# Kernel optimization log

Hardware: AMD Instinct MI355X
Metric: run time of the kernel (lower is better)

## Reference

```python
import jax, jax.numpy as jnp
import numpy as np

N_NODES = 50000
N_EDGES = 625000
IN_DIM = 128
OUT_DIM = 128


def setup_inputs() -> dict:
    key = jax.random.key(0)
    ks = jax.random.split(key, 8)
    feats = jax.random.normal(ks[0], (N_NODES, IN_DIM), dtype=jnp.float32)
    src = jax.random.randint(ks[1], (N_EDGES,), 0, N_NODES, dtype=jnp.int64)
    dst = jax.random.randint(ks[2], (N_EDGES,), 0, N_NODES, dtype=jnp.int64)
    # nn.Linear default init: U(-1/sqrt(fan_in), 1/sqrt(fan_in))
    bf = 1.0 / np.sqrt(IN_DIM)
    W_f = jax.random.uniform(ks[3], (OUT_DIM, IN_DIM), jnp.float32, -bf, bf)
    b_f = jax.random.uniform(ks[4], (OUT_DIM,), jnp.float32, -bf, bf)
    bp = 1.0 / np.sqrt(OUT_DIM)
    W_phy = jax.random.uniform(ks[5], (OUT_DIM, OUT_DIM), jnp.float32, -bp, bp)
    b_phy = jax.random.uniform(ks[6], (OUT_DIM,), jnp.float32, -bp, bp)
    eps = jnp.zeros((1,), dtype=jnp.float32)  # init_eps = 0
    return {"feats": feats, "src": src, "dst": dst, "W_f": W_f, "b_f": b_f,
            "W_phy": W_phy, "b_phy": b_phy, "eps": eps}


def reference(feats, src, dst, W_f, b_f, W_phy, b_phy, eps):
    # mlp_f (num_mlps=1): linear + relu
    h = jax.nn.relu(feats @ W_f.T + b_f)              # [N, out_dim]
    # update_all(copy_u('h'), sum): sum messages h[src] at dst
    n = jax.ops.segment_sum(h[src], dst, num_segments=N_NODES)  # [N, out_dim]
    # faithful to source: h = 1 + eps * h + n
    h = 1.0 + eps * h + n
    # mlp_phy (num_mlps=1): linear + relu
    h = jax.nn.relu(h @ W_phy.T + b_phy)
    return h
```

## Files before the change

kernel.cpp:

```cpp
#include <hip/hip_runtime.h>

#define N_NODES 50000
#define N_EDGES 625000
#define DIM 128
#define CAP 64

typedef __bf16 bf16x8 __attribute__((ext_vector_type(8)));
typedef __bf16 bf16x4 __attribute__((ext_vector_type(4)));
typedef __bf16 bf16x2 __attribute__((ext_vector_type(2)));
typedef float f32x4 __attribute__((ext_vector_type(4)));

__device__ __forceinline__ float bflo(unsigned u) { return __uint_as_float(u << 16); }
__device__ __forceinline__ float bfhi(unsigned u) { return __uint_as_float(u & 0xffff0000u); }

__global__ __launch_bounds__(512) void gemm1_fill_k(
    const float* __restrict__ A_f32,
    const float* __restrict__ W,
    const float* __restrict__ bias,
    __bf16* __restrict__ out_bf16,
    const int* __restrict__ src,
    const int* __restrict__ dst,
    int* __restrict__ cnt,
    int* __restrict__ bucket,
    const float* __restrict__ W_phy,
    __bf16* __restrict__ Wb,
    int gemm_blocks)
{
    const int t = threadIdx.x;

    if ((int)blockIdx.x >= gemm_blocks) {
        if ((int)blockIdx.x == gemm_blocks) {
            if (t < 16) {
                bf16x8 z = {};
                *(bf16x8*)&out_bf16[(size_t)N_NODES * DIM + t * 8] = z;
            }
            for (int i = t; i < 4096; i += 512) {
                float4 f = ((const float4*)W_phy)[i];
                bf16x4 pk = { (__bf16)f.x, (__bf16)f.y, (__bf16)f.z, (__bf16)f.w };
                *(bf16x4*)&Wb[i * 4] = pk;
            }
        }
        int idx = ((int)blockIdx.x - gemm_blocks) * 512 + t;
        if (idx < N_EDGES / 8) {
            int4 sa = ((const int4*)src)[idx * 2];
            int4 sb = ((const int4*)src)[idx * 2 + 1];
            int4 da = ((const int4*)dst)[idx * 2];
            int4 db = ((const int4*)dst)[idx * 2 + 1];
            int p0 = atomicAdd(&cnt[da.x], 1);
            int p1 = atomicAdd(&cnt[da.y], 1);
            int p2 = atomicAdd(&cnt[da.z], 1);
            int p3 = atomicAdd(&cnt[da.w], 1);
            int p4 = atomicAdd(&cnt[db.x], 1);
            int p5 = atomicAdd(&cnt[db.y], 1);
            int p6 = atomicAdd(&cnt[db.z], 1);
            int p7 = atomicAdd(&cnt[db.w], 1);
            bucket[(da.x << 6) + p0] = sa.x;
            bucket[(da.y << 6) + p1] = sa.y;
            bucket[(da.z << 6) + p2] = sa.z;
            bucket[(da.w << 6) + p3] = sa.w;
            bucket[(db.x << 6) + p4] = sb.x;
            bucket[(db.y << 6) + p5] = sb.y;
            bucket[(db.z << 6) + p6] = sb.z;
            bucket[(db.w << 6) + p7] = sb.w;
        }
        return;
    }

    __shared__ __align__(16) __bf16 w_lds[128 * 136];

    for (int i = t; i < 4096; i += 512) {
        float4 f = ((const float4*)W)[i];
        int n = i >> 5;
        int k = (i & 31) << 2;
        bf16x4 pk = { (__bf16)f.x, (__bf16)f.y, (__bf16)f.z, (__bf16)f.w };
        *(bf16x4*)&w_lds[n * 136 + k] = pk;
    }
    __syncthreads();

    const int wave = t >> 6;
    const int lane = t & 63;
    const int q = lane >> 4;
    const int mr = lane & 15;

    const int m0 = blockIdx.x * 128 + wave * 16;
    int arow = m0 + mr;
    if (arow >= N_NODES) arow = N_NODES - 1;

    f32x4 acc[8] = {};

#pragma unroll
    for (int ks = 0; ks < 4; ++ks) {
        const int k0 = ks * 32 + q * 8;
        const float4* ap = (const float4*)&A_f32[(size_t)arow * DIM + k0];
        float4 a0 = ap[0], a1 = ap[1];
        bf16x8 af;
        af[0] = (__bf16)a0.x; af[1] = (__bf16)a0.y;
        af[2] = (__bf16)a0.z; af[3] = (__bf16)a0.w;
        af[4] = (__bf16)a1.x; af[5] = (__bf16)a1.y;
        af[6] = (__bf16)a1.z; af[7] = (__bf16)a1.w;
#pragma unroll
        for (int nt = 0; nt < 8; ++nt) {
            bf16x8 bfr = *(const bf16x8*)&w_lds[(nt * 16 + mr) * 136 + k0];
            acc[nt] = __builtin_amdgcn_mfma_f32_16x16x32_bf16(af, bfr, acc[nt], 0, 0, 0);
        }
    }

    __syncthreads();
    float* lds_f = (float*)w_lds;
    const int nb = blockIdx.x * 128;

#pragma unroll
    for (int half = 0; half < 2; ++half) {
        if ((wave >> 2) == half) {
            int lw = wave & 3;
#pragma unroll
            for (int nt = 0; nt < 8; ++nt)
#pragma unroll
                for (int r = 0; r < 4; ++r)
                    lds_f[(lw * 16 + q * 4 + r) * 132 + nt * 16 + mr] = acc[nt][r];
        }
        __syncthreads();
        for (int i = t; i < 2048; i += 512) {
            int lr = i >> 5;
            int cg = (i & 31) << 2;
            int grow = nb + half * 64 + lr;
            if (grow < N_NODES) {
                float4 v = *(const float4*)&lds_f[lr * 132 + cg];
                float4 b4 = *(const float4*)&bias[cg];
                bf16x4 o;
                o[0] = (__bf16)fmaxf(v.x + b4.x, 0.f);
                o[1] = (__bf16)fmaxf(v.y + b4.y, 0.f);
                o[2] = (__bf16)fmaxf(v.z + b4.z, 0.f);
                o[3] = (__bf16)fmaxf(v.w + b4.w, 0.f);
                *(bf16x4*)&out_bf16[(size_t)grow * DIM + cg] = o;
            }
        }
        __syncthreads();
    }
}

__global__ __launch_bounds__(512, 4) void agg_gemm2_k(
    const __bf16* __restrict__ h,
    const int* __restrict__ cnt,
    const int* __restrict__ bucket,
    const float* __restrict__ eps_p,
    const __bf16* __restrict__ Wb,
    const float* __restrict__ bias,
    float* __restrict__ out)
{
    __shared__ __align__(16) __bf16 lds[2 * 128 * 136];
    __bf16* const w_lds = lds;
    __bf16* const a_lds = lds + 128 * 136;

    const int t = threadIdx.x;

    for (int i = t; i < 2048; i += 512) {
        int n = i >> 4;
        int kk = (i & 15) << 3;
        bf16x8 v = *(const bf16x8*)&Wb[n * DIM + kk];
        *(bf16x8*)&w_lds[n * 136 + kk] = v;
    }

    const int wave = t >> 6;
    const int lane = t & 63;
    const int ch = lane << 1;
    const int rowbase = __builtin_amdgcn_readfirstlane(blockIdx.x * 128 + wave * 16);
    const float eps = eps_p[0];

    int degv[16];
    int idxv[16];
#pragma unroll
    for (int i = 0; i < 16; ++i) {
        const int node = rowbase + i;
        const bool ok = node < N_NODES;
        degv[i] = ok ? cnt[node] : 0;
        idxv[i] = ok ? bucket[(node << 6) | lane] : N_NODES;
    }

#pragma unroll
    for (int i = 0; i < 16; ++i) {
        const int node = rowbase + i;
        const int nd = (node < N_NODES) ? node : N_NODES;
        const int deg = degv[i];
        const unsigned sv = *(const unsigned*)&h[(size_t)nd * DIM + ch];
        const int s = (lane < deg) ? idxv[i] : N_NODES;
        float ax = 0.f, ay = 0.f;
        for (int e = 0; e < deg; e += 8) {
            int s0 = __builtin_amdgcn_readlane(s, e + 0);
            int s1 = __builtin_amdgcn_readlane(s, e + 1);
            int s2 = __builtin_amdgcn_readlane(s, e + 2);
            int s3 = __builtin_amdgcn_readlane(s, e + 3);
            int s4 = __builtin_amdgcn_readlane(s, e + 4);
            int s5 = __builtin_amdgcn_readlane(s, e + 5);
            int s6 = __builtin_amdgcn_readlane(s, e + 6);
            int s7 = __builtin_amdgcn_readlane(s, e + 7);
            unsigned v0 = *(const unsigned*)&h[(size_t)s0 * DIM + ch];
            unsigned v1 = *(const unsigned*)&h[(size_t)s1 * DIM + ch];
            unsigned v2 = *(const unsigned*)&h[(size_t)s2 * DIM + ch];
            unsigned v3 = *(const unsigned*)&h[(size_t)s3 * DIM + ch];
            unsigned v4 = *(const unsigned*)&h[(size_t)s4 * DIM + ch];
            unsigned v5 = *(const unsigned*)&h[(size_t)s5 * DIM + ch];
            unsigned v6 = *(const unsigned*)&h[(size_t)s6 * DIM + ch];
            unsigned v7 = *(const unsigned*)&h[(size_t)s7 * DIM + ch];
            ax += (bflo(v0) + bflo(v1)) + (bflo(v2) + bflo(v3))
                + (bflo(v4) + bflo(v5)) + (bflo(v6) + bflo(v7));
            ay += (bfhi(v0) + bfhi(v1)) + (bfhi(v2) + bfhi(v3))
                + (bfhi(v4) + bfhi(v5)) + (bfhi(v6) + bfhi(v7));
        }
        ax = 1.0f + eps * bflo(sv) + ax;
        ay = 1.0f + eps * bfhi(sv) + ay;
        bf16x2 o; o[0] = (__bf16)ax; o[1] = (__bf16)ay;
        *(bf16x2*)&a_lds[(wave * 16 + i) * 136 + ch] = o;
    }

    __syncthreads();

    const int q = lane >> 4;
    const int mr = lane & 15;

    f32x4 acc[8] = {};

#pragma unroll
    for (int ks = 0; ks < 4; ++ks) {
        const int k0 = ks * 32 + q * 8;
        bf16x8 af = *(const bf16x8*)&a_lds[(wave * 16 + mr) * 136 + k0];
#pragma unroll
        for (int nt = 0; nt < 8; ++nt) {
            bf16x8 bfr = *(const bf16x8*)&w_lds[(nt * 16 + mr) * 136 + k0];
            acc[nt] = __builtin_amdgcn_mfma_f32_16x16x32_bf16(af, bfr, acc[nt], 0, 0, 0);
        }
    }

    __syncthreads();
    float* lds_f = (float*)lds;
    const int nb = blockIdx.x * 128;

#pragma unroll
    for (int half = 0; half < 2; ++half) {
        if ((wave >> 2) == half) {
            int lw = wave & 3;
#pragma unroll
            for (int nt = 0; nt < 8; ++nt)
#pragma unroll
                for (int r = 0; r < 4; ++r)
                    lds_f[(lw * 16 + q * 4 + r) * 132 + nt * 16 + mr] = acc[nt][r];
        }
        __syncthreads();
        for (int i2 = t; i2 < 2048; i2 += 512) {
            int lr = i2 >> 5;
            int cg = (i2 & 31) << 2;
            int grow = nb + half * 64 + lr;
            if (grow < N_NODES) {
                float4 v = *(const float4*)&lds_f[lr * 132 + cg];
                float4 b4 = *(const float4*)&bias[cg];
                v.x = fmaxf(v.x + b4.x, 0.f);
                v.y = fmaxf(v.y + b4.y, 0.f);
                v.z = fmaxf(v.z + b4.z, 0.f);
                v.w = fmaxf(v.w + b4.w, 0.f);
                *(float4*)&out[(size_t)grow * DIM + cg] = v;
            }
        }
        __syncthreads();
    }
}

extern "C" void kernel_launch(void* const* d_in, const int* in_sizes, int n_in,
                              void* d_out, int out_size, void* d_ws, size_t ws_size,
                              hipStream_t stream) {
    const float* feats = (const float*)d_in[0];
    const int*   src   = (const int*)d_in[1];
    const int*   dst   = (const int*)d_in[2];
    const float* W_f   = (const float*)d_in[3];
    const float* b_f   = (const float*)d_in[4];
    const float* W_phy = (const float*)d_in[5];
    const float* b_phy = (const float*)d_in[6];
    const float* eps   = (const float*)d_in[7];
    float* out = (float*)d_out;

    const size_t HN = (size_t)(N_NODES + 1) * DIM;
    __bf16* h   = (__bf16*)d_ws;
    int* bucket = (int*)(h + HN);
    int* cnt    = bucket + (size_t)N_NODES * CAP;
    __bf16* Wb  = (__bf16*)(cnt + N_NODES);

    const int gblocks = (N_NODES + 127) / 128;
    const int fblocks = (N_EDGES / 8 + 511) / 512;

    hipMemsetAsync(cnt, 0, N_NODES * sizeof(int), stream);

    gemm1_fill_k<<<gblocks + fblocks, 512, 0, stream>>>(
        feats, W_f, b_f, h, src, dst, cnt, bucket, W_phy, Wb, gblocks);

    agg_gemm2_k<<<gblocks, 512, 0, stream>>>(
        h, cnt, bucket, eps, Wb, b_phy, out);
}
```

Measured before the change: 152.6 us.

## Split edge bucketing into per-XCD counters with overflow buckets and LDS index compaction

The edge-bucket fill now keeps a separate counter and small 16-slot bucket per XCD for each destination node, read from the hardware XCC_ID register. Entries past that capacity go to a shared overflow bucket with its own atomic counter. The aggregation kernel ballots and compacts the eight per-XCD bucket slices and the overflow entries into a per-wave LDS index list, and prefetches the next node's metadata one step ahead. The aim is to keep atomic contention and cache-line traffic local to each XCD, at the cost of a larger memset, more metadata reads and LDS writes per node.

```diff
diff --git a/kernel.cpp b/kernel.cpp
--- a/kernel.cpp
+++ b/kernel.cpp
@@ -3,7 +3,8 @@
 #define N_NODES 50000
 #define N_EDGES 625000
 #define DIM 128
-#define CAP 64
+#define RCAP 16
+#define OCAP 64
 
 typedef __bf16 bf16x8 __attribute__((ext_vector_type(8)));
 typedef __bf16 bf16x4 __attribute__((ext_vector_type(4)));
@@ -20,8 +21,9 @@
     __bf16* __restrict__ out_bf16,
     const int* __restrict__ src,
     const int* __restrict__ dst,
-    int* __restrict__ cnt,
+    int* __restrict__ cnt9,
     int* __restrict__ bucket,
+    int* __restrict__ obucket,
     const float* __restrict__ W_phy,
     __bf16* __restrict__ Wb,
     int gemm_blocks)
@@ -40,28 +42,41 @@
                 *(bf16x4*)&Wb[i * 4] = pk;
             }
         }
+        int xcd;
+        asm volatile("s_getreg_b32 %0, hwreg(HW_REG_XCC_ID)" : "=s"(xcd));
+        xcd &= 7;
+        const int cb = xcd * N_NODES;
+
         int idx = ((int)blockIdx.x - gemm_blocks) * 512 + t;
         if (idx < N_EDGES / 8) {
             int4 sa = ((const int4*)src)[idx * 2];
             int4 sb = ((const int4*)src)[idx * 2 + 1];
             int4 da = ((const int4*)dst)[idx * 2];
             int4 db = ((const int4*)dst)[idx * 2 + 1];
-            int p0 = atomicAdd(&cnt[da.x], 1);
-            int p1 = atomicAdd(&cnt[da.y], 1);
-            int p2 = atomicAdd(&cnt[da.z], 1);
-            int p3 = atomicAdd(&cnt[da.w], 1);
-            int p4 = atomicAdd(&cnt[db.x], 1);
-            int p5 = atomicAdd(&cnt[db.y], 1);
-            int p6 = atomicAdd(&cnt[db.z], 1);
-            int p7 = atomicAdd(&cnt[db.w], 1);
-            bucket[(da.x << 6) + p0] = sa.x;
-            bucket[(da.y << 6) + p1] = sa.y;
-            bucket[(da.z << 6) + p2] = sa.z;
-            bucket[(da.w << 6) + p3] = sa.w;
-            bucket[(db.x << 6) + p4] = sb.x;
-            bucket[(db.y << 6) + p5] = sb.y;
-            bucket[(db.z << 6) + p6] = sb.z;
-            bucket[(db.w << 6) + p7] = sb.w;
+            int p0 = atomicAdd(&cnt9[cb + da.x], 1);
+            int p1 = atomicAdd(&cnt9[cb + da.y], 1);
+            int p2 = atomicAdd(&cnt9[cb + da.z], 1);
+            int p3 = atomicAdd(&cnt9[cb + da.w], 1);
+            int p4 = atomicAdd(&cnt9[cb + db.x], 1);
+            int p5 = atomicAdd(&cnt9[cb + db.y], 1);
+            int p6 = atomicAdd(&cnt9[cb + db.z], 1);
+            int p7 = atomicAdd(&cnt9[cb + db.w], 1);
+            if (p0 < RCAP) bucket[((cb + da.x) << 4) + p0] = sa.x;
+            else { int q = atomicAdd(&cnt9[8 * N_NODES + da.x], 1); obucket[(da.x << 6) + q] = sa.x; }
+            if (p1 < RCAP) bucket[((cb + da.y) << 4) + p1] = sa.y;
+            else { int q = atomicAdd(&cnt9[8 * N_NODES + da.y], 1); obucket[(da.y << 6) + q] = sa.y; }
+            if (p2 < RCAP) bucket[((cb + da.z) << 4) + p2] = sa.z;
+            else { int q = atomicAdd(&cnt9[8 * N_NODES + da.z], 1); obucket[(da.z << 6) + q] = sa.z; }
+            if (p3 < RCAP) bucket[((cb + da.w) << 4) + p3] = sa.w;
+            else { int q = atomicAdd(&cnt9[8 * N_NODES + da.w], 1); obucket[(da.w << 6) + q] = sa.w; }
+            if (p4 < RCAP) bucket[((cb + db.x) << 4) + p4] = sb.x;
+            else { int q = atomicAdd(&cnt9[8 * N_NODES + db.x], 1); obucket[(db.x << 6) + q] = sb.x; }
+            if (p5 < RCAP) bucket[((cb + db.y) << 4) + p5] = sb.y;
+            else { int q = atomicAdd(&cnt9[8 * N_NODES + db.y], 1); obucket[(db.y << 6) + q] = sb.y; }
+            if (p6 < RCAP) bucket[((cb + db.z) << 4) + p6] = sb.z;
+            else { int q = atomicAdd(&cnt9[8 * N_NODES + db.z], 1); obucket[(db.z << 6) + q] = sb.z; }
+            if (p7 < RCAP) bucket[((cb + db.w) << 4) + p7] = sb.w;
+            else { int q = atomicAdd(&cnt9[8 * N_NODES + db.w], 1); obucket[(db.w << 6) + q] = sb.w; }
         }
         return;
     }
@@ -141,14 +156,16 @@
 
 __global__ __launch_bounds__(512, 4) void agg_gemm2_k(
     const __bf16* __restrict__ h,
-    const int* __restrict__ cnt,
+    const int* __restrict__ cnt9,
     const int* __restrict__ bucket,
+    const int* __restrict__ obucket,
     const float* __restrict__ eps_p,
     const __bf16* __restrict__ Wb,
     const float* __restrict__ bias,
     float* __restrict__ out)
 {
     __shared__ __align__(16) __bf16 lds[2 * 128 * 136];
+    __shared__ __align__(16) int widx_all[8][200];
     __bf16* const w_lds = lds;
     __bf16* const a_lds = lds + 128 * 136;
 
@@ -164,51 +181,68 @@
     const int wave = t >> 6;
     const int lane = t & 63;
     const int ch = lane << 1;
+    const int xq = lane >> 4;
+    const int sj = lane & 15;
     const int rowbase = __builtin_amdgcn_readfirstlane(blockIdx.x * 128 + wave * 16);
     const float eps = eps_p[0];
-
-    int degv[16];
-    int idxv[16];
+    int* const widx = widx_all[wave];
+
+    int ndv[2], cAv[2], cBv[2], rAv[2], rBv[2], ocv[2];
+    unsigned svv[2];
+    auto nload = [&](int sl, int ii) {
+        const int node = rowbase + ii;
+        const int nd = (node < N_NODES) ? node : (N_NODES - 1);
+        ndv[sl] = nd;
+        int ca = cnt9[xq * N_NODES + nd];
+        int cb = cnt9[(xq + 4) * N_NODES + nd];
+        cAv[sl] = (ca < RCAP) ? ca : RCAP;
+        cBv[sl] = (cb < RCAP) ? cb : RCAP;
+        rAv[sl] = bucket[((xq * N_NODES + nd) << 4) + sj];
+        rBv[sl] = bucket[(((xq + 4) * N_NODES + nd) << 4) + sj];
+        ocv[sl] = cnt9[8 * N_NODES + nd];
+        svv[sl] = *(const unsigned*)&h[(size_t)nd * DIM + ch];
+    };
+    nload(0, 0);
+
 #pragma unroll
     for (int i = 0; i < 16; ++i) {
-        const int node = rowbase + i;
-        const bool ok = node < N_NODES;
-        degv[i] = ok ? cnt[node] : 0;
-        idxv[i] = ok ? bucket[(node << 6) | lane] : N_NODES;
-    }
-
-#pragma unroll
-    for (int i = 0; i < 16; ++i) {
-        const int node = rowbase + i;
-        const int nd = (node < N_NODES) ? node : N_NODES;
-        const int deg = degv[i];
-        const unsigned sv = *(const unsigned*)&h[(size_t)nd * DIM + ch];
-        const int s = (lane < deg) ? idxv[i] : N_NODES;
+        if (i < 15) nload((i + 1) & 1, i + 1);
+        const int sl = i & 1;
+        const int nd = ndv[sl];
+
+        const unsigned long long mA = __ballot(sj < cAv[sl]);
+        const unsigned long long mB = __ballot(sj < cBv[sl]);
+        const unsigned long long below = (1ull << lane) - 1ull;
+        const int tA = __popcll(mA);
+        int deg = tA + __popcll(mB);
+        if (sj < cAv[sl]) widx[__popcll(mA & below)] = rAv[sl];
+        if (sj < cBv[sl]) widx[tA + __popcll(mB & below)] = rBv[sl];
+        const int oc = ocv[sl];
+        if (oc > 0) {
+            if (lane < oc) widx[deg + lane] = obucket[(nd << 6) + lane];
+            deg += oc;
+        }
+        if (lane < 8) widx[deg + lane] = N_NODES;
+
         float ax = 0.f, ay = 0.f;
         for (int e = 0; e < deg; e += 8) {
-            int s0 = __builtin_amdgcn_readlane(s, e + 0);
-            int s1 = __builtin_amdgcn_readlane(s, e + 1);
-            int s2 = __builtin_amdgcn_readlane(s, e + 2);
-            int s3 = __builtin_amdgcn_readlane(s, e + 3);
-            int s4 = __builtin_amdgcn_readlane(s, e + 4);
-            int s5 = __builtin_amdgcn_readlane(s, e + 5);
-            int s6 = __builtin_amdgcn_readlane(s, e + 6);
-            int s7 = __builtin_amdgcn_readlane(s, e + 7);
-            unsigned v0 = *(const unsigned*)&h[(size_t)s0 * DIM + ch];
-            unsigned v1 = *(const unsigned*)&h[(size_t)s1 * DIM + ch];
-            unsigned v2 = *(const unsigned*)&h[(size_t)s2 * DIM + ch];
-            unsigned v3 = *(const unsigned*)&h[(size_t)s3 * DIM + ch];
-            unsigned v4 = *(const unsigned*)&h[(size_t)s4 * DIM + ch];
-            unsigned v5 = *(const unsigned*)&h[(size_t)s5 * DIM + ch];
-            unsigned v6 = *(const unsigned*)&h[(size_t)s6 * DIM + ch];
-            unsigned v7 = *(const unsigned*)&h[(size_t)s7 * DIM + ch];
+            int4 w0 = *(const int4*)&widx[e];
+            int4 w1 = *(const int4*)&widx[e + 4];
+            unsigned v0 = *(const unsigned*)&h[(size_t)w0.x * DIM + ch];
+            unsigned v1 = *(const unsigned*)&h[(size_t)w0.y * DIM + ch];
+            unsigned v2 = *(const unsigned*)&h[(size_t)w0.z * DIM + ch];
+            unsigned v3 = *(const unsigned*)&h[(size_t)w0.w * DIM + ch];
+            unsigned v4 = *(const unsigned*)&h[(size_t)w1.x * DIM + ch];
+            unsigned v5 = *(const unsigned*)&h[(size_t)w1.y * DIM + ch];
+            unsigned v6 = *(const unsigned*)&h[(size_t)w1.z * DIM + ch];
+            unsigned v7 = *(const unsigned*)&h[(size_t)w1.w * DIM + ch];
             ax += (bflo(v0) + bflo(v1)) + (bflo(v2) + bflo(v3))
                 + (bflo(v4) + bflo(v5)) + (bflo(v6) + bflo(v7));
             ay += (bfhi(v0) + bfhi(v1)) + (bfhi(v2) + bfhi(v3))
                 + (bfhi(v4) + bfhi(v5)) + (bfhi(v6) + bfhi(v7));
         }
-        ax = 1.0f + eps * bflo(sv) + ax;
-        ay = 1.0f + eps * bfhi(sv) + ay;
+        ax = 1.0f + eps * bflo(svv[sl]) + ax;
+        ay = 1.0f + eps * bfhi(svv[sl]) + ay;
         bf16x2 o; o[0] = (__bf16)ax; o[1] = (__bf16)ay;
         *(bf16x2*)&a_lds[(wave * 16 + i) * 136 + ch] = o;
     }
@@ -278,19 +312,20 @@
     float* out = (float*)d_out;
 
     const size_t HN = (size_t)(N_NODES + 1) * DIM;
-    __bf16* h   = (__bf16*)d_ws;
-    int* bucket = (int*)(h + HN);
-    int* cnt    = bucket + (size_t)N_NODES * CAP;
-    __bf16* Wb  = (__bf16*)(cnt + N_NODES);
+    __bf16* h    = (__bf16*)d_ws;
+    int* bucket  = (int*)(h + HN);
+    int* obucket = bucket + (size_t)8 * N_NODES * RCAP;
+    int* cnt9    = obucket + (size_t)N_NODES * OCAP;
+    __bf16* Wb   = (__bf16*)(cnt9 + (size_t)9 * N_NODES);
 
     const int gblocks = (N_NODES + 127) / 128;
     const int fblocks = (N_EDGES / 8 + 511) / 512;
 
-    hipMemsetAsync(cnt, 0, N_NODES * sizeof(int), stream);
+    hipMemsetAsync(cnt9, 0, (size_t)9 * N_NODES * sizeof(int), stream);
 
     gemm1_fill_k<<<gblocks + fblocks, 512, 0, stream>>>(
-        feats, W_f, b_f, h, src, dst, cnt, bucket, W_phy, Wb, gblocks);
+        feats, W_f, b_f, h, src, dst, cnt9, bucket, obucket, W_phy, Wb, gblocks);
 
     agg_gemm2_k<<<gblocks, 512, 0, stream>>>(
-        h, cnt, bucket, eps, Wb, b_phy, out);
+        h, cnt9, bucket, obucket, eps, Wb, b_phy, out);
 }
```

Result: no change. 154.7 us (+1.4%).

## Replace per-node atomic edge buckets with two-level block-binned edge lists

Applied to the files above, without the earlier changes.

Edge placement no longer does one global atomic per edge into fixed 64-slot per-node buckets. Each fill block now builds a shared-memory histogram of edges by 128-node destination tile and prefix-scans it. It then reserves space with one global atomic per tile and writes packed (local dst, src) words in contiguous runs. The aggregation kernel loads its tile's list into LDS and counting-sorts it per node into 16-bit source indices padded to multiples of 8, then reads them with vector LDS loads instead of readlane. This cuts global atomic traffic and scattered writes, but adds shared-memory scans and sorting, relies on node ids fitting in 16 bits, and silently drops edges past a fixed per-tile capacity.

```diff
diff --git a/kernel.cpp b/kernel.cpp
--- a/kernel.cpp
+++ b/kernel.cpp
@@ -3,7 +3,8 @@
 #define N_NODES 50000
 #define N_EDGES 625000
 #define DIM 128
-#define CAP 64
+#define NB 391
+#define BCAP 2048
 
 typedef __bf16 bf16x8 __attribute__((ext_vector_type(8)));
 typedef __bf16 bf16x4 __attribute__((ext_vector_type(4)));
@@ -20,15 +21,22 @@
     __bf16* __restrict__ out_bf16,
     const int* __restrict__ src,
     const int* __restrict__ dst,
-    int* __restrict__ cnt,
-    int* __restrict__ bucket,
+    unsigned* __restrict__ blist,
+    int* __restrict__ bcnt,
     const float* __restrict__ W_phy,
     __bf16* __restrict__ Wb,
     int gemm_blocks)
 {
+    __shared__ __align__(16) __bf16 smem[128 * 136];
     const int t = threadIdx.x;
 
     if ((int)blockIdx.x >= gemm_blocks) {
+        int* hist       = (int*)smem;
+        int* scanA      = hist + 512;
+        int* rpB        = scanA + 512;
+        int* offB       = rpB + 512;
+        unsigned* stage = (unsigned*)(offB + 512);
+
         if ((int)blockIdx.x == gemm_blocks) {
             if (t < 16) {
                 bf16x8 z = {};
@@ -40,33 +48,69 @@
                 *(bf16x4*)&Wb[i * 4] = pk;
             }
         }
-        int idx = ((int)blockIdx.x - gemm_blocks) * 512 + t;
-        if (idx < N_EDGES / 8) {
+
+        hist[t] = 0;
+        __syncthreads();
+
+        const int idx = ((int)blockIdx.x - gemm_blocks) * 512 + t;
+        const bool valid = idx < N_EDGES / 8;
+        unsigned pk[8];
+        int bk[8];
+        if (valid) {
             int4 sa = ((const int4*)src)[idx * 2];
             int4 sb = ((const int4*)src)[idx * 2 + 1];
             int4 da = ((const int4*)dst)[idx * 2];
             int4 db = ((const int4*)dst)[idx * 2 + 1];
-            int p0 = atomicAdd(&cnt[da.x], 1);
-            int p1 = atomicAdd(&cnt[da.y], 1);
-            int p2 = atomicAdd(&cnt[da.z], 1);
-            int p3 = atomicAdd(&cnt[da.w], 1);
-            int p4 = atomicAdd(&cnt[db.x], 1);
-            int p5 = atomicAdd(&cnt[db.y], 1);
-            int p6 = atomicAdd(&cnt[db.z], 1);
-            int p7 = atomicAdd(&cnt[db.w], 1);
-            bucket[(da.x << 6) + p0] = sa.x;
-            bucket[(da.y << 6) + p1] = sa.y;
-            bucket[(da.z << 6) + p2] = sa.z;
-            bucket[(da.w << 6) + p3] = sa.w;
-            bucket[(db.x << 6) + p4] = sb.x;
-            bucket[(db.y << 6) + p5] = sb.y;
-            bucket[(db.z << 6) + p6] = sb.z;
-            bucket[(db.w << 6) + p7] = sb.w;
+            pk[0] = ((unsigned)(da.x & 127) << 16) | (unsigned)sa.x; bk[0] = da.x >> 7;
+            pk[1] = ((unsigned)(da.y & 127) << 16) | (unsigned)sa.y; bk[1] = da.y >> 7;
+            pk[2] = ((unsigned)(da.z & 127) << 16) | (unsigned)sa.z; bk[2] = da.z >> 7;
+            pk[3] = ((unsigned)(da.w & 127) << 16) | (unsigned)sa.w; bk[3] = da.w >> 7;
+            pk[4] = ((unsigned)(db.x & 127) << 16) | (unsigned)sb.x; bk[4] = db.x >> 7;
+            pk[5] = ((unsigned)(db.y & 127) << 16) | (unsigned)sb.y; bk[5] = db.y >> 7;
+            pk[6] = ((unsigned)(db.z & 127) << 16) | (unsigned)sb.z; bk[6] = db.z >> 7;
+            pk[7] = ((unsigned)(db.w & 127) << 16) | (unsigned)sb.w; bk[7] = db.w >> 7;
+#pragma unroll
+            for (int j = 0; j < 8; ++j) atomicAdd(&hist[bk[j]], 1);
+        }
+        __syncthreads();
+
+        const int hv = hist[t];
+        scanA[t] = hv;
+        __syncthreads();
+        for (int d = 1; d < 512; d <<= 1) {
+            int nv = scanA[t] + ((t >= d) ? scanA[t - d] : 0);
+            __syncthreads();
+            scanA[t] = nv;
+            __syncthreads();
+        }
+        rpB[t] = scanA[t] - hv;
+        offB[t] = scanA[t] - hv;
+        __syncthreads();
+
+        if (valid) {
+#pragma unroll
+            for (int j = 0; j < 8; ++j) {
+                int p = atomicAdd(&offB[bk[j]], 1);
+                stage[p] = pk[j];
+            }
+        }
+        __syncthreads();
+
+        if (t < NB) {
+            int n = hist[t];
+            if (n > 0) {
+                int gb = atomicAdd(&bcnt[t], n);
+                int lim = BCAP - gb;
+                if (n > lim) n = (lim > 0) ? lim : 0;
+                const int base = rpB[t];
+                unsigned* dp = &blist[(size_t)t * BCAP + gb];
+                for (int i2 = 0; i2 < n; ++i2) dp[i2] = stage[base + i2];
+            }
         }
         return;
     }
 
-    __shared__ __align__(16) __bf16 w_lds[128 * 136];
+    __bf16* w_lds = smem;
 
     for (int i = t; i < 4096; i += 512) {
         float4 f = ((const float4*)W)[i];
@@ -141,16 +185,21 @@
 
 __global__ __launch_bounds__(512, 4) void agg_gemm2_k(
     const __bf16* __restrict__ h,
-    const int* __restrict__ cnt,
-    const int* __restrict__ bucket,
+    const unsigned* __restrict__ blist,
+    const int* __restrict__ bcnt,
     const float* __restrict__ eps_p,
     const __bf16* __restrict__ Wb,
     const float* __restrict__ bias,
     float* __restrict__ out)
 {
     __shared__ __align__(16) __bf16 lds[2 * 128 * 136];
+    __shared__ __align__(16) unsigned short slist[3072];
+    __shared__ int histD[128];
+    __shared__ int rp8[128];
+    __shared__ int offD[128];
     __bf16* const w_lds = lds;
     __bf16* const a_lds = lds + 128 * 136;
+    unsigned* const estage = (unsigned*)a_lds;
 
     const int t = threadIdx.x;
 
@@ -161,39 +210,57 @@
         *(bf16x8*)&w_lds[n * 136 + kk] = v;
     }
 
+    int cnt = bcnt[blockIdx.x];
+    if (cnt > BCAP) cnt = BCAP;
+    for (int i = t; i < cnt; i += 512) estage[i] = blist[(size_t)blockIdx.x * BCAP + i];
+    if (t < 128) histD[t] = 0;
+    for (int i = t; i < 3072; i += 512) slist[i] = (unsigned short)N_NODES;
+    __syncthreads();
+
+    for (int i = t; i < cnt; i += 512) atomicAdd(&histD[(estage[i] >> 16) & 127], 1);
+    __syncthreads();
+
+    const int hv = (t < 128) ? ((histD[t] + 7) & ~7) : 0;
+    if (t < 128) rp8[t] = hv;
+    __syncthreads();
+    for (int d = 1; d < 128; d <<= 1) {
+        int nv = 0;
+        if (t < 128) nv = rp8[t] + ((t >= d) ? rp8[t - d] : 0);
+        __syncthreads();
+        if (t < 128) rp8[t] = nv;
+        __syncthreads();
+    }
+    if (t < 128) { int b = rp8[t] - hv; rp8[t] = b; offD[t] = b; }
+    __syncthreads();
+
+    for (int i = t; i < cnt; i += 512) {
+        unsigned e = estage[i];
+        int nl = (e >> 16) & 127;
+        int p = atomicAdd(&offD[nl], 1);
+        slist[p] = (unsigned short)(e & 0xFFFFu);
+    }
+    __syncthreads();
+
     const int wave = t >> 6;
     const int lane = t & 63;
     const int ch = lane << 1;
-    const int rowbase = __builtin_amdgcn_readfirstlane(blockIdx.x * 128 + wave * 16);
+    const int rowbase = blockIdx.x * 128 + wave * 16;
     const float eps = eps_p[0];
 
-    int degv[16];
-    int idxv[16];
-#pragma unroll
     for (int i = 0; i < 16; ++i) {
-        const int node = rowbase + i;
-        const bool ok = node < N_NODES;
-        degv[i] = ok ? cnt[node] : 0;
-        idxv[i] = ok ? bucket[(node << 6) | lane] : N_NODES;
-    }
-
-#pragma unroll
-    for (int i = 0; i < 16; ++i) {
+        const int nl = wave * 16 + i;
         const int node = rowbase + i;
         const int nd = (node < N_NODES) ? node : N_NODES;
-        const int deg = degv[i];
+        const int deg = histD[nl];
+        const int base = rp8[nl];
         const unsigned sv = *(const unsigned*)&h[(size_t)nd * DIM + ch];
-        const int s = (lane < deg) ? idxv[i] : N_NODES;
         float ax = 0.f, ay = 0.f;
         for (int e = 0; e < deg; e += 8) {
-            int s0 = __builtin_amdgcn_readlane(s, e + 0);
-            int s1 = __builtin_amdgcn_readlane(s, e + 1);
-            int s2 = __builtin_amdgcn_readlane(s, e + 2);
-            int s3 = __builtin_amdgcn_readlane(s, e + 3);
-            int s4 = __builtin_amdgcn_readlane(s, e + 4);
-            int s5 = __builtin_amdgcn_readlane(s, e + 5);
-            int s6 = __builtin_amdgcn_readlane(s, e + 6);
-            int s7 = __builtin_amdgcn_readlane(s, e + 7);
+            uint4 w = *(const uint4*)&slist[base + e];
+            int s0 = w.x & 0xFFFF, s1 = w.x >> 16;
+            int s2 = w.y & 0xFFFF, s3 = w.y >> 16;
+            int s4 = w.z & 0xFFFF, s5 = w.z >> 16;
+            int s6 = w.w & 0xFFFF, s7 = w.w >> 16;
             unsigned v0 = *(const unsigned*)&h[(size_t)s0 * DIM + ch];
             unsigned v1 = *(const unsigned*)&h[(size_t)s1 * DIM + ch];
             unsigned v2 = *(const unsigned*)&h[(size_t)s2 * DIM + ch];
@@ -210,7 +277,7 @@
         ax = 1.0f + eps * bflo(sv) + ax;
         ay = 1.0f + eps * bfhi(sv) + ay;
         bf16x2 o; o[0] = (__bf16)ax; o[1] = (__bf16)ay;
-        *(bf16x2*)&a_lds[(wave * 16 + i) * 136 + ch] = o;
+        *(bf16x2*)&a_lds[nl * 136 + ch] = o;
     }
 
     __syncthreads();
@@ -278,19 +345,19 @@
     float* out = (float*)d_out;
 
     const size_t HN = (size_t)(N_NODES + 1) * DIM;
-    __bf16* h   = (__bf16*)d_ws;
-    int* bucket = (int*)(h + HN);
-    int* cnt    = bucket + (size_t)N_NODES * CAP;
-    __bf16* Wb  = (__bf16*)(cnt + N_NODES);
+    __bf16* h       = (__bf16*)d_ws;
+    unsigned* blist = (unsigned*)(h + HN);
+    int* bcnt       = (int*)(blist + (size_t)NB * BCAP);
+    __bf16* Wb      = (__bf16*)(bcnt + 512);
 
     const int gblocks = (N_NODES + 127) / 128;
     const int fblocks = (N_EDGES / 8 + 511) / 512;
 
-    hipMemsetAsync(cnt, 0, N_NODES * sizeof(int), stream);
+    hipMemsetAsync(bcnt, 0, 512 * sizeof(int), stream);
 
     gemm1_fill_k<<<gblocks + fblocks, 512, 0, stream>>>(
-        feats, W_f, b_f, h, src, dst, cnt, bucket, W_phy, Wb, gblocks);
+        feats, W_f, b_f, h, src, dst, blist, bcnt, W_phy, Wb, gblocks);
 
     agg_gemm2_k<<<gblocks, 512, 0, stream>>>(
-        h, cnt, bucket, eps, Wb, b_phy, out);
+        h, blist, bcnt, eps, Wb, b_phy, out);
 }
```

Result: faster. 133.9 us (-12.3%).
